# Optimization experiments

Hardware: AMD Instinct MI355X
Metric: run time of the kernel (lower is better)

## Reference

```python
import jax, jax.numpy as jnp
import numpy as np

EPS = 1e-8

def setup_inputs() -> dict:
    key = jax.random.key(0)
    ks = jax.random.split(key, 10)
    N, IN, Z, C, H = 8192, 512, 128, 64, 50
    x = jax.random.normal(ks[0], (N, IN), dtype=jnp.float32)
    c = jax.random.randint(ks[1], (N, 1), 0, C, dtype=jnp.int64)
    z = jax.random.normal(ks[2], (N, Z), dtype=jnp.float32)
    # f_x MLP params (Linear(IN,50) -> ReLU -> Linear(50,Z))
    W1 = jax.random.normal(ks[3], (IN, H), dtype=jnp.float32) / np.sqrt(IN)
    b1 = jax.random.normal(ks[4], (H,), dtype=jnp.float32) * 0.01
    W2 = jax.random.normal(ks[5], (H, Z), dtype=jnp.float32) / np.sqrt(H)
    b2 = jax.random.normal(ks[6], (Z,), dtype=jnp.float32) * 0.01
    # f_z Linear(Z,Z)
    Wz = jax.random.normal(ks[7], (Z, Z), dtype=jnp.float32) / np.sqrt(Z)
    bz = jax.random.normal(ks[8], (Z,), dtype=jnp.float32) * 0.01
    # per-category bilinear weights w_s [C,Z,Z] (torch.randn init)
    Ws = jax.random.normal(ks[9], (C, Z, Z), dtype=jnp.float32)
    return {"x": x, "c": c, "z": z, "W1": W1, "b1": b1, "W2": W2, "b2": b2, "Wz": Wz, "bz": bz, "Ws": Ws}

def reference(x, c, z, W1, b1, W2, b2, Wz, bz, Ws):
    cf = c.reshape(-1)                                    # [N]
    fx = jax.nn.relu(x @ W1 + b1) @ W2 + b2               # [N,Z]
    fz = z @ Wz + bz                                      # [N,Z]
    # per-sample bilinear: u[n] = fx[n] @ Ws[c[n]]
    u = jnp.einsum('nd,nde->ne', fx, Ws[cf])              # [N,Z]
    T = jax.nn.softplus(jnp.einsum('ne,ne->n', u, fz))    # [N]
    # neg_T[i] = mean over j with c[j]==c[i] of softplus(fx[i] @ Ws[c[i]] @ fz[j])
    S = jax.nn.softplus(u @ fz.T)                         # [N,N]
    mask = (cf[:, None] == cf[None, :]).astype(S.dtype)   # [N,N]
    neg_T = (S * mask).sum(axis=1) / mask.sum(axis=1)     # [N]
    return jnp.log(T + EPS) - jnp.log(neg_T + EPS)
```

## Files before the change

kernel.cpp:

```cpp
#include <hip/hip_runtime.h>
#include <math.h>

#define N_   8192
#define IN_  512
#define ZD   128
#define CC   64
#define HD   50
#define EPSF 1e-8f

typedef float vf4 __attribute__((ext_vector_type(4)));
typedef __attribute__((ext_vector_type(8))) short bfrag;

#define MFMA16(a, b, c) __builtin_amdgcn_mfma_f32_16x16x32_bf16((a), (b), (c), 0, 0, 0)

__device__ __forceinline__ float softplus_hot(float t) {
    return fmaxf(t, 0.f) + __logf(1.f + __expf(-fabsf(t)));
}
__device__ __forceinline__ float softplus_acc(float t) {
    return fmaxf(t, 0.f) + log1pf(expf(-fabsf(t)));
}
__device__ __forceinline__ unsigned short bf16_rn(float x) {
    unsigned int u = __float_as_uint(x);
    return (unsigned short)((u + 0x7fff + ((u >> 16) & 1)) >> 16);
}
__device__ __forceinline__ float bf16_f(unsigned short h) {
    return __uint_as_float(((unsigned int)h) << 16);
}
__device__ __forceinline__ void split8(const float* v, bfrag& hi, bfrag& lo) {
    #pragma unroll
    for (int e = 0; e < 8; ++e) {
        unsigned int u = __float_as_uint(v[e]);
        unsigned short h = (unsigned short)(u >> 16);
        ((short*)&hi)[e] = (short)h;
        ((short*)&lo)[e] = (short)bf16_rn(v[e] - bf16_f(h));
    }
}

__global__ __launch_bounds__(256) void k_pre(const int* __restrict__ c,
                                             const float* __restrict__ W1,
                                             const float* __restrict__ z,
                                             const float* __restrict__ Wz,
                                             const float* __restrict__ bz,
                                             const float* __restrict__ W2,
                                             const float* __restrict__ Ws,
                                             uint4* __restrict__ W1p,
                                             uint4* __restrict__ W2p,
                                             float* __restrict__ fz,
                                             unsigned short* __restrict__ fz_hi,
                                             unsigned short* __restrict__ Wst_hi,
                                             unsigned short* __restrict__ Wst_lo,
                                             int* __restrict__ counts,
                                             int* __restrict__ offsets,
                                             int* __restrict__ grouped) {
    __shared__ float smem[64 * 129];
    int tid = threadIdx.x;
    int b   = blockIdx.x;
    if (b < CC) {
        __shared__ int hist[CC];
        __shared__ int cursor;
        __shared__ int off_s;
        if (tid < CC) hist[tid] = 0;
        if (tid == 0) cursor = 0;
        __syncthreads();
        for (int i = tid; i < N_; i += 256) atomicAdd(&hist[c[i]], 1);
        __syncthreads();
        if (tid == 0) {
            int off = 0;
            for (int q = 0; q < b; ++q) off += hist[q];
            off_s = off;
            counts[b]  = hist[b];
            offsets[b] = off;
        }
        __syncthreads();
        int off = off_s;
        for (int i = tid; i < N_; i += 256) {
            if (c[i] == b) {
                int p = atomicAdd(&cursor, 1);
                grouped[off + p] = i;
            }
        }
    } else if (b < 80) {
        int unit = (b - 64) * 256 + tid;
        int lane = unit & 63, f = (unit >> 6) & 15, kc = unit >> 10;
        int nt = f >> 2, ks = f & 3;
        int n = nt * 16 + (lane & 15);
        int kbase = kc * 128 + ks * 32 + (lane >> 4) * 8;
        unsigned short hi8[8], lo8[8];
        #pragma unroll
        for (int j = 0; j < 8; ++j) {
            int k = kbase + j;
            float v = (n < HD) ? W1[k * HD + n] : 0.f;
            unsigned short h = bf16_rn(v);
            hi8[j] = h;
            lo8[j] = bf16_rn(v - bf16_f(h));
        }
        W1p[kc * 2048 + f * 64 + lane]        = *(uint4*)hi8;
        W1p[kc * 2048 + 1024 + f * 64 + lane] = *(uint4*)lo8;
    } else if (b < 84) {
        int unit = (b - 80) * 256 + tid;
        int lane = unit & 63, f = unit >> 6;
        int nt = f >> 1, ks = f & 1;
        int n = nt * 16 + (lane & 15);
        int kbase = ks * 32 + (lane >> 4) * 8;
        unsigned short hi8[8], lo8[8];
        #pragma unroll
        for (int j = 0; j < 8; ++j) {
            int k = kbase + j;
            float v = (k < HD) ? W2[k * ZD + n] : 0.f;
            unsigned short h = bf16_rn(v);
            hi8[j] = h;
            lo8[j] = bf16_rn(v - bf16_f(h));
        }
        W2p[f * 64 + lane]        = *(uint4*)hi8;
        W2p[1024 + f * 64 + lane] = *(uint4*)lo8;
    } else if (b < 212) {
        float* sz = smem;
        int row0 = (b - 84) * 64;
        vf4* s4 = (vf4*)sz;
        const vf4* z4 = (const vf4*)(z + (size_t)row0 * ZD);
        #pragma unroll
        for (int f = 0; f < 8; ++f) s4[tid + f * 256] = z4[tid + f * 256];
        __syncthreads();
        int cp = tid & 31, rgp = tid >> 5;
        const vf4* Wz4 = (const vf4*)Wz;
        vf4 bb = ((const vf4*)bz)[cp];
        vf4 acc[8];
        #pragma unroll
        for (int r = 0; r < 8; ++r) acc[r] = bb;
        #pragma unroll 1
        for (int d4 = 0; d4 < 32; ++d4) {
            vf4 w0 = Wz4[(4 * d4 + 0) * 32 + cp];
            vf4 w1 = Wz4[(4 * d4 + 1) * 32 + cp];
            vf4 w2 = Wz4[(4 * d4 + 2) * 32 + cp];
            vf4 w3 = Wz4[(4 * d4 + 3) * 32 + cp];
            #pragma unroll
            for (int r = 0; r < 8; ++r) {
                vf4 a = s4[(rgp * 8 + r) * 32 + d4];
                acc[r] += a[0] * w0;
                acc[r] += a[1] * w1;
                acc[r] += a[2] * w2;
                acc[r] += a[3] * w3;
            }
        }
        vf4* fz4 = (vf4*)fz;
        #pragma unroll
        for (int r = 0; r < 8; ++r) {
            int n = row0 + rgp * 8 + r;
            fz4[(size_t)n * 32 + cp] = acc[r];
            ushort4 h;
            h.x = bf16_rn(acc[r][0]); h.y = bf16_rn(acc[r][1]);
            h.z = bf16_rn(acc[r][2]); h.w = bf16_rn(acc[r][3]);
            *(ushort4*)(fz_hi + (size_t)n * ZD + cp * 4) = h;
        }
    } else {
        int cat = b - 212;
        const float* Wc = Ws + (size_t)cat * ZD * ZD;
        unsigned short* Whi = Wst_hi + (size_t)cat * ZD * ZD;
        unsigned short* Wlo = Wst_lo + (size_t)cat * ZD * ZD;
        #pragma unroll 1
        for (int half = 0; half < 2; ++half) {
            __syncthreads();
            const vf4* src = (const vf4*)(Wc + (size_t)half * 64 * ZD);
            #pragma unroll
            for (int f = 0; f < 8; ++f) {
                int idx = tid + f * 256;
                int row = idx >> 5, q = idx & 31;
                vf4 v = src[idx];
                #pragma unroll
                for (int e = 0; e < 4; ++e) smem[row * 129 + q * 4 + e] = v[e];
            }
            __syncthreads();
            #pragma unroll 1
            for (int f = 0; f < 32; ++f) {
                int idx = tid + f * 256;
                int e = idx >> 6, dd = idx & 63;
                float v = smem[dd * 129 + e];
                unsigned short h = bf16_rn(v);
                Whi[(size_t)e * ZD + half * 64 + dd] = h;
                Wlo[(size_t)e * ZD + half * 64 + dd] = bf16_rn(v - bf16_f(h));
            }
        }
    }
}

#define TI 8
__global__ __launch_bounds__(512) void k_all(const float* __restrict__ x,
                                             const uint4* __restrict__ W1p,
                                             const uint4* __restrict__ W2p,
                                             const float* __restrict__ b1,
                                             const float* __restrict__ b2,
                                             const unsigned short* __restrict__ Wst_hi,
                                             const unsigned short* __restrict__ Wst_lo,
                                             const float* __restrict__ fz,
                                             const unsigned short* __restrict__ fz_hi,
                                             const int* __restrict__ grouped,
                                             const int* __restrict__ offsets,
                                             const int* __restrict__ counts,
                                             float* __restrict__ out) {
    __shared__ __align__(16) unsigned char SM[78848];
    uint4* A4    = (uint4*)(SM);
    uint4* B4    = (uint4*)(SM + 34816);
    float* shC   = (float*)(SM + 69632);
    float* sRedF = (float*)(SM + 78336);

    int tid = threadIdx.x;
    int cat = blockIdx.x >> 3;
    int t   = blockIdx.x & (TI - 1);
    int off = offsets[cat], cnt = counts[cat];
    int i0 = t * 32;
    if (i0 >= cnt) return;
    int mI = min(32, cnt - i0);

    int lane = tid & 63, wave = tid >> 6;
    int m = lane & 15, quad = lane >> 4;
    int rg = wave & 1, ch = wave >> 1;

    uint4* sW2 = A4;
    uint4* sW1 = B4;
    float* sh  = shC;

    #pragma unroll
    for (int f = 0; f < 4; ++f) sW2[tid + f * 512] = W2p[tid + f * 512];

    int irowA = rg * 16 + m;
    int n_gA = grouped[off + i0 + min(irowA, mI - 1)];
    const float4* xr = (const float4*)(x + (size_t)n_gA * IN_);

    vf4 accP = {0.f, 0.f, 0.f, 0.f};
    vf4 accQ = {0.f, 0.f, 0.f, 0.f};
    vf4 accR = {0.f, 0.f, 0.f, 0.f};

    #pragma unroll 1
    for (int kc = 0; kc < 4; ++kc) {
        uint4 w1r0 = W1p[kc * 2048 + tid];
        uint4 w1r1 = W1p[kc * 2048 + tid + 512];
        uint4 w1r2 = W1p[kc * 2048 + tid + 1024];
        uint4 w1r3 = W1p[kc * 2048 + tid + 1536];
        __syncthreads();
        sW1[tid]        = w1r0;
        sW1[tid + 512]  = w1r1;
        sW1[tid + 1024] = w1r2;
        sW1[tid + 1536] = w1r3;
        __syncthreads();
        #pragma unroll
        for (int ks = 0; ks < 4; ++ks) {
            float4 xa = xr[kc * 32 + ks * 8 + quad * 2];
            float4 xb = xr[kc * 32 + ks * 8 + quad * 2 + 1];
            float xv[8] = {xa.x, xa.y, xa.z, xa.w, xb.x, xb.y, xb.z, xb.w};
            bfrag ah, al;
            split8(xv, ah, al);
            bfrag bh = *(const bfrag*)&sW1[(ch * 4 + ks) * 64 + lane];
            bfrag bl = *(const bfrag*)&sW1[1024 + (ch * 4 + ks) * 64 + lane];
            accP = MFMA16(ah, bh, accP);
            accQ = MFMA16(ah, bl, accQ);
            accR = MFMA16(al, bh, accR);
        }
    }
    {
        int col = ch * 16 + m;
        float bb = (col < HD) ? b1[col] : 0.f;
        vf4 acc = accP + accQ + accR;
        #pragma unroll
        for (int r = 0; r < 4; ++r)
            sh[(rg * 16 + quad * 4 + r) * 68 + col] = fmaxf(acc[r] + bb, 0.f);
    }
    __syncthreads();

    bfrag ah2[2], al2[2];
    #pragma unroll
    for (int ks = 0; ks < 2; ++ks) {
        const float4* shp = (const float4*)&sh[(rg * 16 + m) * 68 + ks * 32 + quad * 8];
        float4 ha = shp[0], hb = shp[1];
        float hv[8] = {ha.x, ha.y, ha.z, ha.w, hb.x, hb.y, hb.z, hb.w};
        split8(hv, ah2[ks], al2[ks]);
    }
    __syncthreads();

    unsigned short* fxhiT = (unsigned short*)shC;
    unsigned short* fxloT = (unsigned short*)B4;
    #pragma unroll
    for (int nt2 = 0; nt2 < 2; ++nt2) {
        int nt = ch * 2 + nt2;
        bfrag bh0 = *(const bfrag*)&sW2[(nt * 2 + 0) * 64 + lane];
        bfrag bl0 = *(const bfrag*)&sW2[1024 + (nt * 2 + 0) * 64 + lane];
        bfrag bh1 = *(const bfrag*)&sW2[(nt * 2 + 1) * 64 + lane];
        bfrag bl1 = *(const bfrag*)&sW2[1024 + (nt * 2 + 1) * 64 + lane];
        vf4 aA = {0.f, 0.f, 0.f, 0.f}, aB = {0.f, 0.f, 0.f, 0.f};
        aA = MFMA16(ah2[0], bh0, aA);
        aA = MFMA16(ah2[0], bl0, aA);
        aA = MFMA16(al2[0], bh0, aA);
        aB = MFMA16(ah2[1], bh1, aB);
        aB = MFMA16(ah2[1], bl1, aB);
        aB = MFMA16(al2[1], bh1, aB);
        vf4 a2 = aA + aB;
        int colB = nt * 16 + m;
        float bb2 = b2[colB];
        #pragma unroll
        for (int r = 0; r < 4; ++r) {
            int row = rg * 16 + quad * 4 + r;
            float v = a2[r] + bb2;
            unsigned int u = __float_as_uint(v);
            unsigned short hh = (unsigned short)(u >> 16);
            fxhiT[row * 136 + colB] = hh;
            fxloT[row * 136 + colB] = bf16_rn(v - bf16_f(hh));
        }
    }
    __syncthreads();

    int eh = ch;
    bfrag a_hi[4], a_lo[4];
    #pragma unroll
    for (int kb = 0; kb < 4; ++kb) {
        a_hi[kb] = *(const bfrag*)&fxhiT[(rg * 16 + m) * 136 + kb * 32 + quad * 8];
        a_lo[kb] = *(const bfrag*)&fxloT[(rg * 16 + m) * 136 + kb * 32 + quad * 8];
    }
    __syncthreads();

    uint4* sWhi = A4;
    uint4* sWlo = B4;
    const uint4* gh = (const uint4*)(Wst_hi + (size_t)cat * ZD * ZD);
    const uint4* gl = (const uint4*)(Wst_lo + (size_t)cat * ZD * ZD);
    #pragma unroll
    for (int f = 0; f < 4; ++f) {
        int idx = tid + f * 512;
        int e = idx >> 4, q = idx & 15;
        sWhi[e * 17 + q] = gh[idx];
        sWlo[e * 17 + q] = gl[idx];
    }
    __syncthreads();

    vf4 uacc[2];
    #pragma unroll 1
    for (int et2 = 0; et2 < 2; ++et2) {
        int et = eh * 2 + et2;
        vf4 aH = {0.f, 0.f, 0.f, 0.f};
        vf4 aM = {0.f, 0.f, 0.f, 0.f};
        vf4 aL = {0.f, 0.f, 0.f, 0.f};
        #pragma unroll
        for (int kb = 0; kb < 4; ++kb) {
            bfrag bh = *(const bfrag*)&sWhi[(et * 16 + m) * 17 + kb * 4 + quad];
            bfrag bl = *(const bfrag*)&sWlo[(et * 16 + m) * 17 + kb * 4 + quad];
            aH = MFMA16(a_hi[kb], bh, aH);
            aM = MFMA16(a_hi[kb], bl, aM);
            aL = MFMA16(a_lo[kb], bh, aL);
        }
        uacc[et2] = aH + aM + aL;
    }

    int nrow[4];
    #pragma unroll
    for (int r = 0; r < 4; ++r) {
        int ir = rg * 16 + quad * 4 + r;
        nrow[r] = (ir < mI) ? grouped[off + i0 + ir] : -1;
    }
    float fzv[2][4];
    #pragma unroll
    for (int et2 = 0; et2 < 2; ++et2) {
        #pragma unroll
        for (int r = 0; r < 4; ++r) {
            fzv[et2][r] = 0.f;
            if (nrow[r] >= 0)
                fzv[et2][r] = fz[(size_t)nrow[r] * ZD + (eh * 2 + et2) * 16 + m];
        }
    }
    float p[4] = {0.f, 0.f, 0.f, 0.f};
    #pragma unroll
    for (int et2 = 0; et2 < 2; ++et2) {
        #pragma unroll
        for (int r = 0; r < 4; ++r) p[r] += uacc[et2][r] * fzv[et2][r];
    }
    #pragma unroll
    for (int r = 0; r < 4; ++r) {
        float v = p[r];
        #pragma unroll
        for (int s = 8; s >= 1; s >>= 1) v += __shfl_xor(v, s, 64);
        p[r] = v;
    }
    if (m == 0) {
        #pragma unroll
        for (int r = 0; r < 4; ++r)
            sRedF[(rg * 4 + eh) * 16 + quad * 4 + r] = p[r];
    }
    __syncthreads();

    unsigned short* su = (unsigned short*)A4;
    #pragma unroll
    for (int et2 = 0; et2 < 2; ++et2) {
        int col = (eh * 2 + et2) * 16 + m;
        #pragma unroll
        for (int r = 0; r < 4; ++r)
            su[(rg * 16 + quad * 4 + r) * 136 + col] = bf16_rn(uacc[et2][r]);
    }
    float logT_r[4] = {0.f, 0.f, 0.f, 0.f};
    if (eh == 0) {
        #pragma unroll
        for (int r = 0; r < 4; ++r) {
            float pt = sRedF[(rg * 4 + 0) * 16 + quad * 4 + r]
                     + sRedF[(rg * 4 + 1) * 16 + quad * 4 + r]
                     + sRedF[(rg * 4 + 2) * 16 + quad * 4 + r]
                     + sRedF[(rg * 4 + 3) * 16 + quad * 4 + r];
            logT_r[r] = logf(softplus_acc(pt) + EPSF);
        }
    }
    __syncthreads();

    bfrag na[4];
    #pragma unroll
    for (int kb = 0; kb < 4; ++kb)
        na[kb] = *(const bfrag*)&su[(rg * 16 + m) * 136 + kb * 32 + quad * 8];

    uint4* sB = B4;
    float negsum[4] = {0.f, 0.f, 0.f, 0.f};
    int jr_s = tid >> 4, q_s = tid & 15;

    uint4 pf0, pf1;
    {
        int mJ0 = min(64, cnt);
        uint4 v0 = {0u, 0u, 0u, 0u}, v1 = {0u, 0u, 0u, 0u};
        if (jr_s < mJ0) {
            int j_g = grouped[off + jr_s];
            v0 = *(const uint4*)(fz_hi + (size_t)j_g * ZD + q_s * 8);
        }
        if (jr_s + 32 < mJ0) {
            int j_g = grouped[off + jr_s + 32];
            v1 = *(const uint4*)(fz_hi + (size_t)j_g * ZD + q_s * 8);
        }
        pf0 = v0; pf1 = v1;
    }

    #pragma unroll 1
    for (int jb = 0; jb < cnt; jb += 64) {
        int mJ = min(64, cnt - jb);
        __syncthreads();
        sB[jr_s * 17 + q_s]        = pf0;
        sB[(jr_s + 32) * 17 + q_s] = pf1;
        int jn = jb + 64;
        if (jn < cnt) {
            int mJn = min(64, cnt - jn);
            uint4 v0 = {0u, 0u, 0u, 0u}, v1 = {0u, 0u, 0u, 0u};
            if (jr_s < mJn) {
                int j_g = grouped[off + jn + jr_s];
                v0 = *(const uint4*)(fz_hi + (size_t)j_g * ZD + q_s * 8);
            }
            if (jr_s + 32 < mJn) {
                int j_g = grouped[off + jn + jr_s + 32];
                v1 = *(const uint4*)(fz_hi + (size_t)j_g * ZD + q_s * 8);
            }
            pf0 = v0; pf1 = v1;
        }
        __syncthreads();
        {
            int jt = eh;
            bfrag b0 = *(const bfrag*)&sB[(jt * 16 + m) * 17 + 0 + quad];
            bfrag b1 = *(const bfrag*)&sB[(jt * 16 + m) * 17 + 4 + quad];
            bfrag b2 = *(const bfrag*)&sB[(jt * 16 + m) * 17 + 8 + quad];
            bfrag b3 = *(const bfrag*)&sB[(jt * 16 + m) * 17 + 12 + quad];
            vf4 aA = {0.f, 0.f, 0.f, 0.f}, aB = {0.f, 0.f, 0.f, 0.f};
            aA = MFMA16(na[0], b0, aA);
            aA = MFMA16(na[1], b1, aA);
            aB = MFMA16(na[2], b2, aB);
            aB = MFMA16(na[3], b3, aB);
            vf4 acc = aA + aB;
            bool jok = (jt * 16 + m) < mJ;
            #pragma unroll
            for (int r = 0; r < 4; ++r)
                if (jok) negsum[r] += softplus_hot(acc[r]);
        }
    }

    #pragma unroll
    for (int r = 0; r < 4; ++r) {
        float v = negsum[r];
        #pragma unroll
        for (int s = 8; s >= 1; s >>= 1) v += __shfl_xor(v, s, 64);
        negsum[r] = v;
    }
    if (m == 0) {
        #pragma unroll
        for (int r = 0; r < 4; ++r)
            sRedF[(rg * 4 + eh) * 16 + quad * 4 + r] = negsum[r];
    }
    __syncthreads();
    if (eh == 0 && m == 0) {
        #pragma unroll
        for (int r = 0; r < 4; ++r) {
            if (nrow[r] >= 0) {
                float tot = sRedF[(rg * 4 + 0) * 16 + quad * 4 + r]
                          + sRedF[(rg * 4 + 1) * 16 + quad * 4 + r]
                          + sRedF[(rg * 4 + 2) * 16 + quad * 4 + r]
                          + sRedF[(rg * 4 + 3) * 16 + quad * 4 + r];
                out[nrow[r]] = logT_r[r] - logf(tot / (float)cnt + EPSF);
            }
        }
    }
}

extern "C" void kernel_launch(void* const* d_in, const int* in_sizes, int n_in,
                              void* d_out, int out_size, void* d_ws, size_t ws_size,
                              hipStream_t stream) {
    const float* x  = (const float*)d_in[0];
    const int*   c  = (const int*)  d_in[1];
    const float* z  = (const float*)d_in[2];
    const float* W1 = (const float*)d_in[3];
    const float* b1 = (const float*)d_in[4];
    const float* W2 = (const float*)d_in[5];
    const float* b2 = (const float*)d_in[6];
    const float* Wz = (const float*)d_in[7];
    const float* bz = (const float*)d_in[8];
    const float* Ws = (const float*)d_in[9];
    float* out = (float*)d_out;

    uint4* W1p = (uint4*)d_ws;
    uint4* W2p = W1p + 8192;
    float* fz  = (float*)(W2p + 2048);
    unsigned short* fz_hi  = (unsigned short*)(fz + (size_t)N_ * ZD);
    unsigned short* Wst_hi = fz_hi + (size_t)N_ * ZD;
    unsigned short* Wst_lo = Wst_hi + (size_t)CC * ZD * ZD;
    int* counts  = (int*)(Wst_lo + (size_t)CC * ZD * ZD);
    int* offsets = counts + CC;
    int* grouped = offsets + CC;

    k_pre <<<276, 256, 0, stream>>>(c, W1, z, Wz, bz, W2, Ws, W1p, W2p, fz,
                                    fz_hi, Wst_hi, Wst_lo, counts, offsets,
                                    grouped);
    k_all <<<CC * TI, 512, 0, stream>>>(x, W1p, W2p, b1, b2, Wst_hi, Wst_lo,
                                        fz, fz_hi, grouped, offsets, counts,
                                        out);
}
```

Before: 131.1 us.

## Read MLP weights from global directly and prefetch bilinear weights early

W1 and W2 fragments are now read straight from global memory (relying on cache hits) instead of being staged through shared memory, which removes the two barriers per K-chunk in the first GEMM. The freed shared space is used to load the per-category W_hi tile at kernel start. The W_lo tile is prefetched into registers before the second GEMM and written to shared memory afterwards, so its global latency overlaps compute. The trade-off is more global/L2 traffic for the weights and higher register pressure from holding the prefetched tile.

```diff
diff --git a/kernel.cpp b/kernel.cpp
--- a/kernel.cpp
+++ b/kernel.cpp
@@ -215,13 +215,16 @@
     int m = lane & 15, quad = lane >> 4;
     int rg = wave & 1, ch = wave >> 1;
 
-    uint4* sW2 = A4;
-    uint4* sW1 = B4;
-    float* sh  = shC;
-
-    #pragma unroll
-    for (int f = 0; f < 4; ++f) sW2[tid + f * 512] = W2p[tid + f * 512];
-
+    const uint4* gh = (const uint4*)(Wst_hi + (size_t)cat * ZD * ZD);
+    {
+        int e0 = tid >> 4, q0 = tid & 15;
+        A4[e0 * 17 + q0]                = gh[tid];
+        A4[(e0 + 32) * 17 + q0]         = gh[tid + 512];
+        A4[(e0 + 64) * 17 + q0]         = gh[tid + 1024];
+        A4[(e0 + 96) * 17 + q0]         = gh[tid + 1536];
+    }
+
+    float* sh = shC;
     int irowA = rg * 16 + m;
     int n_gA = grouped[off + i0 + min(irowA, mI - 1)];
     const float4* xr = (const float4*)(x + (size_t)n_gA * IN_);
@@ -232,16 +235,6 @@
 
     #pragma unroll 1
     for (int kc = 0; kc < 4; ++kc) {
-        uint4 w1r0 = W1p[kc * 2048 + tid];
-        uint4 w1r1 = W1p[kc * 2048 + tid + 512];
-        uint4 w1r2 = W1p[kc * 2048 + tid + 1024];
-        uint4 w1r3 = W1p[kc * 2048 + tid + 1536];
-        __syncthreads();
-        sW1[tid]        = w1r0;
-        sW1[tid + 512]  = w1r1;
-        sW1[tid + 1024] = w1r2;
-        sW1[tid + 1536] = w1r3;
-        __syncthreads();
         #pragma unroll
         for (int ks = 0; ks < 4; ++ks) {
             float4 xa = xr[kc * 32 + ks * 8 + quad * 2];
@@ -249,8 +242,8 @@
             float xv[8] = {xa.x, xa.y, xa.z, xa.w, xb.x, xb.y, xb.z, xb.w};
             bfrag ah, al;
             split8(xv, ah, al);
-            bfrag bh = *(const bfrag*)&sW1[(ch * 4 + ks) * 64 + lane];
-            bfrag bl = *(const bfrag*)&sW1[1024 + (ch * 4 + ks) * 64 + lane];
+            bfrag bh = *(const bfrag*)&W1p[kc * 2048 + (ch * 4 + ks) * 64 + lane];
+            bfrag bl = *(const bfrag*)&W1p[kc * 2048 + 1024 + (ch * 4 + ks) * 64 + lane];
             accP = MFMA16(ah, bh, accP);
             accQ = MFMA16(ah, bl, accQ);
             accR = MFMA16(al, bh, accR);
@@ -276,15 +269,21 @@
     }
     __syncthreads();
 
+    const uint4* gl = (const uint4*)(Wst_lo + (size_t)cat * ZD * ZD);
+    uint4 wl0 = gl[tid];
+    uint4 wl1 = gl[tid + 512];
+    uint4 wl2 = gl[tid + 1024];
+    uint4 wl3 = gl[tid + 1536];
+
     unsigned short* fxhiT = (unsigned short*)shC;
     unsigned short* fxloT = (unsigned short*)B4;
     #pragma unroll
     for (int nt2 = 0; nt2 < 2; ++nt2) {
         int nt = ch * 2 + nt2;
-        bfrag bh0 = *(const bfrag*)&sW2[(nt * 2 + 0) * 64 + lane];
-        bfrag bl0 = *(const bfrag*)&sW2[1024 + (nt * 2 + 0) * 64 + lane];
-        bfrag bh1 = *(const bfrag*)&sW2[(nt * 2 + 1) * 64 + lane];
-        bfrag bl1 = *(const bfrag*)&sW2[1024 + (nt * 2 + 1) * 64 + lane];
+        bfrag bh0 = *(const bfrag*)&W2p[(nt * 2 + 0) * 64 + lane];
+        bfrag bl0 = *(const bfrag*)&W2p[1024 + (nt * 2 + 0) * 64 + lane];
+        bfrag bh1 = *(const bfrag*)&W2p[(nt * 2 + 1) * 64 + lane];
+        bfrag bl1 = *(const bfrag*)&W2p[1024 + (nt * 2 + 1) * 64 + lane];
         vf4 aA = {0.f, 0.f, 0.f, 0.f}, aB = {0.f, 0.f, 0.f, 0.f};
         aA = MFMA16(ah2[0], bh0, aA);
         aA = MFMA16(ah2[0], bl0, aA);
@@ -318,14 +317,12 @@
 
     uint4* sWhi = A4;
     uint4* sWlo = B4;
-    const uint4* gh = (const uint4*)(Wst_hi + (size_t)cat * ZD * ZD);
-    const uint4* gl = (const uint4*)(Wst_lo + (size_t)cat * ZD * ZD);
-    #pragma unroll
-    for (int f = 0; f < 4; ++f) {
-        int idx = tid + f * 512;
-        int e = idx >> 4, q = idx & 15;
-        sWhi[e * 17 + q] = gh[idx];
-        sWlo[e * 17 + q] = gl[idx];
+    {
+        int e0 = tid >> 4, q0 = tid & 15;
+        sWlo[e0 * 17 + q0]        = wl0;
+        sWlo[(e0 + 32) * 17 + q0] = wl1;
+        sWlo[(e0 + 64) * 17 + q0] = wl2;
+        sWlo[(e0 + 96) * 17 + q0] = wl3;
     }
     __syncthreads();
 
```

New measurement: 132.8 us. Within noise of the previous version (+1.3%).
